# Optimization experiments

Measured on AMD Instinct MI355X. Metric: run time of the kernel, lower is better.

The kernel has to match this reference:

```python
import jax, jax.numpy as jnp
import numpy as np
from jax import lax

KERNEL_EPS = 1e-4   # eps in softmax_kernel
ATTN_EPS = 1e-6     # eps in causal_linear_attention
CHUNK = 64          # chunk length for the causal scan


def softmax_kernel(data, projection_matrix, is_query):
    # data: [b,h,n,d], projection_matrix: [r,d]
    d = data.shape[-1]
    r = projection_matrix.shape[0]
    data_normalizer = d ** -0.25
    ratio = r ** -0.5
    data_dash = jnp.einsum('bhnd,rd->bhnr', data_normalizer * data, projection_matrix)
    diag_data = (jnp.sum(data ** 2, axis=-1) * 0.5 * data_normalizer ** 2)[..., None]  # [b,h,n,1]
    if is_query:
        stab = jnp.max(data_dash, axis=-1, keepdims=True)
    else:
        stab = jnp.max(data_dash)
    return ratio * (jnp.exp(data_dash - diag_data - stab) + KERNEL_EPS)


def causal_linear_attention(qp, kp, v, chunk=CHUNK, eps=ATTN_EPS):
    # qp,kp: [b,h,n,r] feature maps; v: [b,h,n,e]
    b, h, n, r = qp.shape
    e = v.shape[-1]
    nc = n // chunk
    # -> [nc, b, h, chunk, *] for lax.scan over chunks
    qs = jnp.moveaxis(qp.reshape(b, h, nc, chunk, r), 2, 0)
    ks = jnp.moveaxis(kp.reshape(b, h, nc, chunk, r), 2, 0)
    vs = jnp.moveaxis(v.reshape(b, h, nc, chunk, e), 2, 0)

    def step(carry, xs):
        k_last, ctx_last = carry  # [b,h,r], [b,h,r,e]
        qch, kch, vch = xs        # [b,h,c,r], [b,h,c,r], [b,h,c,e]
        k_cum = k_last[:, :, None, :] + jnp.cumsum(kch, axis=2)              # [b,h,c,r]
        D_inv = 1.0 / jnp.einsum('bhcr,bhcr->bhc', qch, k_cum + eps)         # [b,h,c]
        ctx = jnp.einsum('bhcr,bhce->bhcre', kch, vch)                       # [b,h,c,r,e]
        ctx_cum = ctx_last[:, :, None] + jnp.cumsum(ctx, axis=2)             # [b,h,c,r,e]
        out = jnp.einsum('bhcre,bhcr,bhc->bhce', ctx_cum, qch, D_inv)        # [b,h,c,e]
        return (k_cum[:, :, -1], ctx_cum[:, :, -1]), out

    init = (jnp.zeros((b, h, r), qp.dtype), jnp.zeros((b, h, r, e), qp.dtype))
    _, outs = lax.scan(step, init, (qs, ks, vs))  # outs: [nc,b,h,c,e]
    return jnp.moveaxis(outs, 0, 2).reshape(b, h, n, e)


def setup_inputs() -> dict:
    key = jax.random.key(0)
    kq, kk, kv, kp = jax.random.split(key, 4)
    b, h, n, d, r = 2, 8, 4096, 64, 256
    q = jax.random.normal(kq, (b, h, n, d), dtype=jnp.float32)
    k = jax.random.normal(kk, (b, h, n, d), dtype=jnp.float32)
    v = jax.random.normal(kv, (b, h, n, d), dtype=jnp.float32)
    projection_matrix = jax.random.normal(kp, (r, d), dtype=jnp.float32)
    return {"q": q, "k": k, "v": v, "projection_matrix": projection_matrix}


def reference(q, k, v, projection_matrix):
    qp = softmax_kernel(q, projection_matrix, is_query=True)
    kp = softmax_kernel(k, projection_matrix, is_query=False)
    return causal_linear_attention(qp, kp, v)
```

## Files before the change

kernel.cpp:

```cpp
#include <hip/hip_runtime.h>


typedef unsigned short ushort_t;
typedef __attribute__((ext_vector_type(8))) short bf16x8;
typedef __attribute__((ext_vector_type(4))) float f32x4;

#define KEPS 1e-4f
#define AEPS 1e-6f
#define NORMIZER 0.35355339059327373f
#define RATIO 0.0625f

__device__ __forceinline__ ushort_t bf16r(float f) {
  unsigned u = __float_as_uint(f);
  return (ushort_t)((u + 0x7fffu + ((u >> 16) & 1u)) >> 16);
}
__device__ __forceinline__ float ubf(ushort_t h) {
  return __uint_as_float((unsigned)h << 16);
}

__global__ __launch_bounds__(256) void pconv_kernel(
    const float* __restrict__ P, ushort_t* __restrict__ Phi,
    ushort_t* __restrict__ Plo)
{
  int idx = blockIdx.x * 1024 + threadIdx.x;
  #pragma unroll
  for (int p = 0; p < 4; ++p) {
    int i = idx + p * 256;
    float x = P[i];
    ushort_t h = bf16r(x);
    Phi[i] = h;
    Plo[i] = bf16r(x - ubf(h));
  }
}

__device__ __forceinline__ void stage_ptile(const ushort_t* __restrict__ gt,
                                            ushort_t* lds0, int tid) {
  int wv = tid >> 6, lane = tid & 63;
  #pragma unroll
  for (int i = 0; i < 2; ++i) {
    int D = i * 256 + wv * 64 + lane;
    int row = D >> 3, c3 = D & 7;
    int sc = (row << 3) | (c3 ^ (row & 7));
    __builtin_amdgcn_global_load_lds(
        (const __attribute__((address_space(1))) void*)(gt + sc * 8),
        (__attribute__((address_space(3))) void*)(lds0 + (i * 256 + wv * 64) * 8),
        16, 0, 0);
  }
}

__global__ __launch_bounds__(256, 3) void feat_mfma(
    const float* __restrict__ Q, const float* __restrict__ K,
    const float* __restrict__ V,
    const ushort_t* __restrict__ Phi, const ushort_t* __restrict__ Plo,
    ushort_t* __restrict__ qp, ushort_t* __restrict__ E,
    float* __restrict__ bmax,
    ushort_t* __restrict__ SE, float* __restrict__ zE,
    float* __restrict__ SV)
{
  __shared__ union {
    struct {
      ushort_t Xhi[64 * 72];
      ushort_t Xlo[64 * 72];
      ushort_t Pt[2][4096];
    } s;
    ushort_t outb[64 * 268];
    ushort_t Et[256 * 72];
  } u;
  __shared__ ushort_t Vt[64 * 72];
  __shared__ float red2[256];
  __shared__ float diagS[64];
  __shared__ float redm[4];

  int bid = blockIdx.x, tid = threadIdx.x;
  bool isK = bid >= 1024;
  int bc = bid - 1024;
  const float* X = isK ? K : Q;
  size_t rowbase = (size_t)(isK ? bc : bid) * 64;

  stage_ptile(Phi, &u.s.Pt[0][0], tid);

  float vv[16];
  if (isK) {
    #pragma unroll
    for (int p = 0; p < 16; ++p)
      vv[p] = V[rowbase * 64 + tid + p * 256];
  }

  #pragma unroll
  for (int p = 0; p < 4; ++p) {
    int idx = tid + p * 256;
    int row = idx >> 4, c4 = idx & 15;
    float4 x = *(const float4*)&X[(rowbase + row) * 64 + c4 * 4];
    ushort4 h, l;
    h.x = bf16r(x.x); l.x = bf16r(x.x - ubf(h.x));
    h.y = bf16r(x.y); l.y = bf16r(x.y - ubf(h.y));
    h.z = bf16r(x.z); l.z = bf16r(x.z - ubf(h.z));
    h.w = bf16r(x.w); l.w = bf16r(x.w - ubf(h.w));
    *(ushort4*)&u.s.Xhi[row * 72 + c4 * 4] = h;
    *(ushort4*)&u.s.Xlo[row * 72 + c4 * 4] = l;
    float ss = x.x * x.x + x.y * x.y + x.z * x.z + x.w * x.w;
    ss += __shfl_xor(ss, 1, 64); ss += __shfl_xor(ss, 2, 64);
    ss += __shfl_xor(ss, 4, 64); ss += __shfl_xor(ss, 8, 64);
    if ((tid & 15) == 0) diagS[row] = 0.0625f * ss;
  }
  __syncthreads();

  int lane = tid & 63, wv = tid >> 6;
  int n15 = lane & 15, quad = lane >> 4;

  bf16x8 ah[2], al[2];
  #pragma unroll
  for (int ks = 0; ks < 2; ++ks) {
    int off = (16 * wv + n15) * 72 + quad * 8 + 32 * ks;
    ah[ks] = *(const bf16x8*)&u.s.Xhi[off];
    al[ks] = *(const bf16x8*)&u.s.Xlo[off];
  }

  f32x4 acc[16];
  #pragma unroll
  for (int tc = 0; tc < 16; ++tc) acc[tc] = f32x4{0.f, 0.f, 0.f, 0.f};

  int buf = 0;
  #pragma unroll
  for (int t = 0; t < 8; ++t) {
    int q4 = t >> 1;
    bool isLo = t & 1;
    if (t) {
      asm volatile("s_waitcnt vmcnt(0)" ::: "memory");
      __builtin_amdgcn_s_barrier();
    }
    if (t < 7) {
      int tn = t + 1;
      const ushort_t* gt = ((tn & 1) ? Plo : Phi) + (size_t)(tn >> 1) * 4096;
      stage_ptile(gt, &u.s.Pt[buf ^ 1][0], tid);
    }
    #pragma unroll
    for (int tcl = 0; tcl < 4; ++tcl) {
      f32x4 a = acc[q4 * 4 + tcl];
      #pragma unroll
      for (int ks = 0; ks < 2; ++ks) {
        int jr = 16 * tcl + n15;
        int rc = (quad + 4 * ks) ^ (n15 & 7);
        bf16x8 b = *(const bf16x8*)&u.s.Pt[buf][jr * 64 + rc * 8];
        a = __builtin_amdgcn_mfma_f32_16x16x32_bf16(ah[ks], b, a, 0, 0, 0);
        if (!isLo)
          a = __builtin_amdgcn_mfma_f32_16x16x32_bf16(al[ks], b, a, 0, 0, 0);
      }
      acc[q4 * 4 + tcl] = a;
    }
    buf ^= 1;
  }

  float dg[4];
  #pragma unroll
  for (int r = 0; r < 4; ++r) dg[r] = diagS[16 * wv + quad * 4 + r];

  float sub[4];
  if (!isK) {
    #pragma unroll
    for (int r = 0; r < 4; ++r) {
      float mx = -3.0e38f;
      #pragma unroll
      for (int tc = 0; tc < 16; ++tc) mx = fmaxf(mx, acc[tc][r]);
      #pragma unroll
      for (int s = 1; s < 16; s <<= 1) mx = fmaxf(mx, __shfl_xor(mx, s, 64));
      sub[r] = dg[r] + NORMIZER * mx;
    }
  } else {
    float bm = -3.0e38f;
    #pragma unroll
    for (int tc = 0; tc < 16; ++tc)
      #pragma unroll
      for (int r = 0; r < 4; ++r) bm = fmaxf(bm, acc[tc][r]);
    #pragma unroll
    for (int s = 1; s < 64; s <<= 1) bm = fmaxf(bm, __shfl_xor(bm, s, 64));
    if (lane == 0) redm[wv] = bm;
    #pragma unroll
    for (int r = 0; r < 4; ++r) sub[r] = dg[r];
  }

  unsigned hp[16][2];
  __syncthreads();
  ushort_t* dst = (isK ? E : qp) + rowbase * 256;
  #pragma unroll
  for (int tc = 0; tc < 16; ++tc) {
    #pragma unroll
    for (int r = 0; r < 4; ++r) {
      int row = 16 * wv + quad * 4 + r;
      float ex = __expf(NORMIZER * acc[tc][r] - sub[r]);
      float val = isK ? ex : RATIO * (ex + KEPS);
      ushort_t h = bf16r(val);
      u.outb[row * 268 + 16 * tc + n15] = h;
      if (r & 1) hp[tc][r >> 1] |= ((unsigned)h << 16);
      else       hp[tc][r >> 1] = (unsigned)h;
    }
  }
  __syncthreads();
  #pragma unroll
  for (int p = 0; p < 8; ++p) {
    int g = (tid + p * 256) * 8;
    int row = g >> 8, c0 = g & 255;
    bf16x8 v0 = *(const bf16x8*)&u.outb[row * 268 + c0];
    *(bf16x8*)&dst[row * 256 + c0] = v0;
  }

  if (isK && tid == 0) {
    float m4 = fmaxf(fmaxf(redm[0], redm[1]), fmaxf(redm[2], redm[3]));
    bmax[bc] = NORMIZER * m4;
  }

  if (!isK) return;

  __syncthreads();

  float vsum = 0.f;
  #pragma unroll
  for (int p = 0; p < 16; ++p) {
    int g = tid + p * 256;
    int pos = g >> 6, e = g & 63;
    float x = vv[p];
    vsum += x;
    int pr = (pos + 8 * ((e >> 3) & 7)) & 63;
    Vt[e * 72 + pr] = bf16r(x);
  }
  red2[tid] = vsum;

  #pragma unroll
  for (int tc = 0; tc < 16; ++tc) {
    int j = 16 * tc + n15;
    int rot = 8 * ((j >> 3) & 7);
    int pw = (16 * wv + quad * 4 + rot) & 63;
    ushort4 w4;
    w4.x = (ushort_t)(hp[tc][0] & 0xffffu);
    w4.y = (ushort_t)(hp[tc][0] >> 16);
    w4.z = (ushort_t)(hp[tc][1] & 0xffffu);
    w4.w = (ushort_t)(hp[tc][1] >> 16);
    *(ushort4*)&u.Et[j * 72 + pw] = w4;
  }
  __syncthreads();

  if (tid < 64)
    SV[(size_t)bc * 64 + tid] =
        red2[tid] + red2[64 + tid] + red2[128 + tid] + red2[192 + tid];

  {
    float s = 0.f;
    #pragma unroll
    for (int m8 = 0; m8 < 8; ++m8) {
      bf16x8 r8 = *(const bf16x8*)&u.Et[tid * 72 + m8 * 8];
      #pragma unroll
      for (int x = 0; x < 8; ++x) s += ubf((ushort_t)r8[x]);
    }
    zE[(size_t)bc * 256 + tid] = s;
  }

  bf16x8 aV[2];
  {
    int e = 16 * wv + n15;
    int rot = 8 * ((e >> 3) & 7);
    #pragma unroll
    for (int ks = 0; ks < 2; ++ks) {
      int pr = (quad * 8 + 32 * ks + rot) & 63;
      aV[ks] = *(const bf16x8*)&Vt[e * 72 + pr];
    }
  }

  f32x4 acc2[16];
  #pragma unroll
  for (int tc = 0; tc < 16; ++tc) {
    int j = 16 * tc + n15;
    int rot = 8 * ((j >> 3) & 7);
    f32x4 a = {0.f, 0.f, 0.f, 0.f};
    #pragma unroll
    for (int ks = 0; ks < 2; ++ks) {
      int pr = (quad * 8 + 32 * ks + rot) & 63;
      bf16x8 b = *(const bf16x8*)&u.Et[j * 72 + pr];
      a = __builtin_amdgcn_mfma_f32_16x16x32_bf16(aV[ks], b, a, 0, 0, 0);
    }
    acc2[tc] = a;
  }
  __syncthreads();

  #pragma unroll
  for (int tc = 0; tc < 16; ++tc)
    #pragma unroll
    for (int r = 0; r < 4; ++r) {
      int e = 16 * wv + quad * 4 + r;
      u.outb[e * 268 + 16 * tc + n15] = bf16r(acc2[tc][r]);
    }
  __syncthreads();
  ushort_t* sdst = SE + rowbase * 256;
  #pragma unroll
  for (int p = 0; p < 8; ++p) {
    int g = (tid + p * 256) * 8;
    int e = g >> 8, j0 = g & 255;
    bf16x8 v0 = *(const bf16x8*)&u.outb[e * 268 + j0];
    *(bf16x8*)&sdst[e * 256 + j0] = v0;
  }
}

__global__ __launch_bounds__(256) void kmax_reduce(
    const float* __restrict__ bmax, float* __restrict__ kmax)
{
  __shared__ float red[4];
  int tid = threadIdx.x;
  float m = fmaxf(fmaxf(bmax[tid], bmax[tid + 256]),
                  fmaxf(bmax[tid + 512], bmax[tid + 768]));
  #pragma unroll
  for (int s = 1; s < 64; s <<= 1) m = fmaxf(m, __shfl_xor(m, s, 64));
  if ((tid & 63) == 0) red[tid >> 6] = m;
  __syncthreads();
  if (tid == 0)
    *kmax = fmaxf(fmaxf(red[0], red[1]), fmaxf(red[2], red[3]));
}

__global__ __launch_bounds__(256) void prefix_kernel(
    ushort_t* __restrict__ S, float* __restrict__ zE,
    const float* __restrict__ SV, const float* __restrict__ kmax)
{
  int b = blockIdx.x;
  float m = *kmax;
  float c1 = RATIO * __expf(-m);
  const float c0 = RATIO * KEPS;
  if (b < 1024) {
    int flat = b * 256 + threadIdx.x;
    int bh = flat >> 14;
    int idx = flat & 16383;
    int e = idx >> 8;
    size_t base = (size_t)bh * 1048576 + idx;
    const float* svp = SV + (size_t)bh * 4096 + e;
    float runE = 0.f, runV = 0.f;
    for (int cc = 0; cc < 64; cc += 8) {
      ushort_t t[8]; float sv[8];
      #pragma unroll
      for (int u2 = 0; u2 < 8; ++u2) {
        t[u2] = S[base + (size_t)(cc + u2) * 16384];
        sv[u2] = svp[(size_t)(cc + u2) * 64];
      }
      #pragma unroll
      for (int u2 = 0; u2 < 8; ++u2) {
        S[base + (size_t)(cc + u2) * 16384] = bf16r(c1 * runE + c0 * runV);
        runE += ubf(t[u2]);
        runV += sv[u2];
      }
    }
  } else {
    int bh = b - 1024;
    int j = threadIdx.x;
    size_t base = (size_t)bh * 16384 + j;
    float run = 0.f;
    for (int cc = 0; cc < 64; cc += 8) {
      float t[8];
      #pragma unroll
      for (int u2 = 0; u2 < 8; ++u2)
        t[u2] = zE[base + (size_t)(cc + u2) * 256];
      #pragma unroll
      for (int u2 = 0; u2 < 8; ++u2) {
        zE[base + (size_t)(cc + u2) * 256] = run;
        run += c1 * t[u2] + 64.0f * c0;
      }
    }
  }
}

__device__ __forceinline__ void stage_tile(const ushort_t* __restrict__ gt,
                                           ushort_t* lds0, int tid, int wv) {
  #pragma unroll
  for (int i = 0; i < 2; ++i) {
    int D = i * 256 + tid;
    int row = D >> 5, cl = D & 31;
    int sc = (row << 5) | (cl ^ (row & 7));
    __builtin_amdgcn_global_load_lds(
        (const __attribute__((address_space(1))) void*)(gt + sc * 8),
        (__attribute__((address_space(3))) void*)(lds0 + (i * 256 + wv * 64) * 8),
        16, 0, 0);
  }
}

__global__ __launch_bounds__(256) void fused_mfma(
    const ushort_t* __restrict__ qp, const ushort_t* __restrict__ E,
    const float* __restrict__ kmax, const float* __restrict__ Z,
    const ushort_t* __restrict__ S, const float* __restrict__ V,
    float* __restrict__ out)
{
  __shared__ ushort_t As[64 * 72];
  __shared__ ushort_t Vt[64 * 72];
  __shared__ ushort_t Bst[2][4096];
  __shared__ float zv[256];
  __shared__ float qsumS[64];
  __shared__ float dqS[64];

  int bc = blockIdx.x, tid = threadIdx.x;
  int lane = tid & 63, wv = tid >> 6;
  int n15 = lane & 15, quad = lane >> 4;
  float m = *kmax;
  float c1 = RATIO * __expf(-m);
  const float c0 = RATIO * KEPS;
  size_t base = (size_t)bc * 16384;

  zv[tid] = Z[(size_t)bc * 256 + tid] + AEPS;
  #pragma unroll
  for (int p = 0; p < 16; ++p) {
    int idx = tid + p * 256;
    int t = idx >> 6, e = idx & 63;
    Vt[e * 72 + t] = bf16r(V[(size_t)bc * 4096 + idx]);
  }
  __syncthreads();

  stage_tile(E + base, &Bst[0][0], tid, wv);

  bf16x8 aQ[8];
  #pragma unroll
  for (int ks = 0; ks < 8; ++ks)
    aQ[ks] = *(const bf16x8*)&qp[base + (size_t)(16 * wv + n15) * 256 + quad * 8 + 32 * ks];

  float qsum = 0.f, dq = 0.f;
  #pragma unroll
  for (int ks = 0; ks < 8; ++ks)
    #pragma unroll
    for (int j = 0; j < 8; ++j) {
      float qv = ubf((ushort_t)aQ[ks][j]);
      qsum += qv;
      dq += qv * zv[quad * 8 + 32 * ks + j];
    }
  qsum += __shfl_xor(qsum, 16, 64); qsum += __shfl_xor(qsum, 32, 64);
  dq   += __shfl_xor(dq, 16, 64);   dq   += __shfl_xor(dq, 32, 64);
  if (quad == 0) { qsumS[16 * wv + n15] = qsum; dqS[16 * wv + n15] = dq; }

  float rs[4] = {0.f, 0.f, 0.f, 0.f};
  float dinv[4] = {0.f, 0.f, 0.f, 0.f};

  #pragma unroll
  for (int t = 0; t < 8; ++t) {
    asm volatile("s_waitcnt vmcnt(0)" ::: "memory");
    __builtin_amdgcn_s_barrier();
    if (t < 7) {
      const ushort_t* gt = (t < 3) ? (E + base + (size_t)(t + 1) * 4096)
                                   : (S + base + (size_t)(t - 3) * 4096);
      stage_tile(gt, &Bst[(t + 1) & 1][0], tid, wv);
    }

    bf16x8 bf[8];
    #pragma unroll
    for (int ks = 0; ks < 8; ++ks) {
      int rc = (4 * ks + quad) ^ (n15 & 7);
      bf[ks] = *(const bf16x8*)&Bst[t & 1][(n15 * 32 + rc) * 8];
    }
    f32x4 g = {0.f, 0.f, 0.f, 0.f};
    #pragma unroll
    for (int ks = 0; ks < 8; ++ks)
      g = __builtin_amdgcn_mfma_f32_16x16x32_bf16(aQ[ks], bf[ks], g, 0, 0, 0);

    if (t < 4) {
      int tc = t;
      #pragma unroll
      for (int r = 0; r < 4; ++r) {
        int i = 16 * wv + quad * 4 + r;
        int tt = 16 * tc + n15;
        float val = (tt <= i) ? (c1 * g[r] + c0 * qsumS[i]) : 0.f;
        As[i * 72 + tt] = bf16r(val);
        rs[r] += val;
      }
      if (t == 3) {
        #pragma unroll
        for (int r = 0; r < 4; ++r) {
          float v2 = rs[r];
          #pragma unroll
          for (int s = 1; s < 16; s <<= 1) v2 += __shfl_xor(v2, s, 64);
          int i = 16 * wv + quad * 4 + r;
          dinv[r] = 1.f / (dqS[i] + v2);
        }
      }
    } else {
      int ec = t - 4;
      f32x4 o = g;
      #pragma unroll
      for (int ks = 0; ks < 2; ++ks) {
        bf16x8 a2 = *(const bf16x8*)&As[(16 * wv + n15) * 72 + quad * 8 + 32 * ks];
        bf16x8 b2 = *(const bf16x8*)&Vt[(16 * ec + n15) * 72 + quad * 8 + 32 * ks];
        o = __builtin_amdgcn_mfma_f32_16x16x32_bf16(a2, b2, o, 0, 0, 0);
      }
      #pragma unroll
      for (int r = 0; r < 4; ++r) {
        int i = 16 * wv + quad * 4 + r;
        out[(size_t)bc * 4096 + (size_t)i * 64 + 16 * ec + n15] = o[r] * dinv[r];
      }
    }
  }
}

extern "C" void kernel_launch(void* const* d_in, const int* in_sizes, int n_in,
                              void* d_out, int out_size, void* d_ws, size_t ws_size,
                              hipStream_t stream)
{
  const float* q = (const float*)d_in[0];
  const float* k = (const float*)d_in[1];
  const float* v = (const float*)d_in[2];
  const float* P = (const float*)d_in[3];
  float* out = (float*)d_out;

  ushort_t* qp  = (ushort_t*)d_ws;
  ushort_t* E   = qp + 16777216;
  ushort_t* S   = E + 16777216;
  float*    zE  = (float*)(S + 16777216);
  float*    SV  = zE + 262144;
  ushort_t* Phi = (ushort_t*)(SV + 65536);
  ushort_t* Plo = Phi + 16384;
  float*    bmax = (float*)(Plo + 16384);
  float*    kmax = bmax + 1024;

  pconv_kernel<<<16, 256, 0, stream>>>(P, Phi, Plo);
  feat_mfma<<<2048, 256, 0, stream>>>(q, k, v, Phi, Plo, qp, E, bmax,
                                      S, zE, SV);
  kmax_reduce<<<1, 256, 0, stream>>>(bmax, kmax);
  prefix_kernel<<<1040, 256, 0, stream>>>(S, zE, SV, kmax);
  fused_mfma<<<1024, 256, 0, stream>>>(qp, E, kmax, zE, S, v, out);
}
```

Before: 166.8 us.

## Load V directly into MFMA operand layout, drop Vt/red2 LDS, raise occupancy

V is now loaded from global memory straight into the bf16 MFMA A-operand registers. The column sums come from wave shuffles instead of an LDS transpose buffer and a reduction array. Removing the Vt and red2 shared arrays shrinks LDS, and the launch bound is raised to 4 blocks per CU. K blocks are also reordered to come first in the grid. The costs are strided, uncoalesced global loads of V and possible register pressure or spills under the tighter occupancy bound.

```diff
diff --git a/kernel.cpp b/kernel.cpp
--- a/kernel.cpp
+++ b/kernel.cpp
@@ -48,7 +48,7 @@
   }
 }
 
-__global__ __launch_bounds__(256, 3) void feat_mfma(
+__global__ __launch_bounds__(256, 4) void feat_mfma(
     const float* __restrict__ Q, const float* __restrict__ K,
     const float* __restrict__ V,
     const ushort_t* __restrict__ Phi, const ushort_t* __restrict__ Plo,
@@ -66,24 +66,29 @@
     ushort_t outb[64 * 268];
     ushort_t Et[256 * 72];
   } u;
-  __shared__ ushort_t Vt[64 * 72];
-  __shared__ float red2[256];
   __shared__ float diagS[64];
   __shared__ float redm[4];
 
   int bid = blockIdx.x, tid = threadIdx.x;
-  bool isK = bid >= 1024;
-  int bc = bid - 1024;
+  bool isK = bid < 1024;
+  int bc = bid;
   const float* X = isK ? K : Q;
-  size_t rowbase = (size_t)(isK ? bc : bid) * 64;
+  size_t rowbase = (size_t)(isK ? bid : bid - 1024) * 64;
+
+  int lane = tid & 63, wv = tid >> 6;
+  int n15 = lane & 15, quad = lane >> 4;
 
   stage_ptile(Phi, &u.s.Pt[0][0], tid);
 
-  float vv[16];
+  float vraw[16];
   if (isK) {
     #pragma unroll
-    for (int p = 0; p < 16; ++p)
-      vv[p] = V[rowbase * 64 + tid + p * 256];
+    for (int ks = 0; ks < 2; ++ks)
+      #pragma unroll
+      for (int jj = 0; jj < 8; ++jj) {
+        int pos = quad * 8 + 32 * ks + jj;
+        vraw[ks * 8 + jj] = V[rowbase * 64 + (size_t)pos * 64 + 16 * wv + n15];
+      }
   }
 
   #pragma unroll
@@ -103,10 +108,24 @@
     ss += __shfl_xor(ss, 4, 64); ss += __shfl_xor(ss, 8, 64);
     if ((tid & 15) == 0) diagS[row] = 0.0625f * ss;
   }
-  __syncthreads();
-
-  int lane = tid & 63, wv = tid >> 6;
-  int n15 = lane & 15, quad = lane >> 4;
+
+  bf16x8 aV[2];
+  if (isK) {
+    float vsum = 0.f;
+    #pragma unroll
+    for (int ks = 0; ks < 2; ++ks)
+      #pragma unroll
+      for (int jj = 0; jj < 8; ++jj) {
+        float x = vraw[ks * 8 + jj];
+        vsum += x;
+        aV[ks][jj] = (short)bf16r(x);
+      }
+    vsum += __shfl_xor(vsum, 16, 64);
+    vsum += __shfl_xor(vsum, 32, 64);
+    if (quad == 0) SV[(size_t)bc * 64 + 16 * wv + n15] = vsum;
+  }
+
+  __syncthreads();
 
   bf16x8 ah[2], al[2];
   #pragma unroll
@@ -212,18 +231,6 @@
   if (!isK) return;
 
   __syncthreads();
-
-  float vsum = 0.f;
-  #pragma unroll
-  for (int p = 0; p < 16; ++p) {
-    int g = tid + p * 256;
-    int pos = g >> 6, e = g & 63;
-    float x = vv[p];
-    vsum += x;
-    int pr = (pos + 8 * ((e >> 3) & 7)) & 63;
-    Vt[e * 72 + pr] = bf16r(x);
-  }
-  red2[tid] = vsum;
 
   #pragma unroll
   for (int tc = 0; tc < 16; ++tc) {
@@ -239,10 +246,6 @@
   }
   __syncthreads();
 
-  if (tid < 64)
-    SV[(size_t)bc * 64 + tid] =
-        red2[tid] + red2[64 + tid] + red2[128 + tid] + red2[192 + tid];
-
   {
     float s = 0.f;
     #pragma unroll
@@ -252,17 +255,6 @@
       for (int x = 0; x < 8; ++x) s += ubf((ushort_t)r8[x]);
     }
     zE[(size_t)bc * 256 + tid] = s;
-  }
-
-  bf16x8 aV[2];
-  {
-    int e = 16 * wv + n15;
-    int rot = 8 * ((e >> 3) & 7);
-    #pragma unroll
-    for (int ks = 0; ks < 2; ++ks) {
-      int pr = (quad * 8 + 32 * ks + rot) & 63;
-      aV[ks] = *(const bf16x8*)&Vt[e * 72 + pr];
-    }
   }
 
   f32x4 acc2[16];
```

New measurement: 157.5 us. 1.06x faster.
